# Kernel optimization log

Measured on AMD Instinct MI355X. Metric: run time of the kernel, lower is better.

Reference implementation:

```python
import jax, jax.numpy as jnp
import numpy as np

N_HOSTS = 16
N_WINDOW = 3
GAT_IN = 3
D = 16          # d_model = gat_output_feats = n_hosts
NHEAD = 2
HD = D // NHEAD # 8
FF = 64
PROTO_DIM = 8
LATENT = N_HOSTS * D * N_WINDOW  # 768
LN_EPS = 1e-5


def _positional_encoding():
    pos = np.arange(N_WINDOW, dtype=np.float32)[:, None]
    div = np.exp(np.arange(0, D, 2, dtype=np.float32) * (-np.log(10000.0) / D))
    pe = np.zeros((N_WINDOW, D), dtype=np.float32)
    pe[:, 0::2] = np.sin(pos * div)
    pe[:, 1::2] = np.cos(pos * div)
    return jnp.asarray(pe[:, None, :])  # (n_window, 1, d_model)


def setup_inputs() -> dict:
    key = jax.random.key(0)
    ks = iter(jax.random.split(key, 40))
    p = lambda *s: jax.random.normal(next(ks), s, dtype=jnp.float32) * 0.05
    inp = {
        't': jax.random.normal(next(ks), (N_WINDOW * N_HOSTS * GAT_IN,), dtype=jnp.float32),
        's': jax.random.normal(next(ks), (N_HOSTS, PROTO_DIM), dtype=jnp.float32),
        # GAT (single head, fully connected 16-node graph)
        'gat_W': p(GAT_IN, D), 'gat_a_src': p(D), 'gat_a_dst': p(D),
        # time encoder Linear(16,16)
        'te_W': p(D, D), 'te_b': p(D),
        'pe': _positional_encoding(),
        # 2 transformer encoder layers, stacked on leading axis
        'qkv_W': p(2, 3 * D, D), 'qkv_b': p(2, 3 * D),
        'out_W': p(2, D, D), 'out_b': p(2, D),
        'ln1_g': jnp.ones((2, D), jnp.float32), 'ln1_b': jnp.zeros((2, D), jnp.float32),
        'ff1_W': p(2, FF, D), 'ff1_b': p(2, FF),
        'ff2_W': p(2, D, FF), 'ff2_b': p(2, D),
        'ln2_g': jnp.ones((2, D), jnp.float32), 'ln2_b': jnp.zeros((2, D), jnp.float32),
        # decoder heads
        'an_W': p(2 * N_HOSTS, LATENT), 'an_b': p(2 * N_HOSTS),
        'pr_W': p(PROTO_DIM * N_HOSTS, LATENT), 'pr_b': p(PROTO_DIM * N_HOSTS),
    }
    return inp


def _layer_norm(x, g, b):
    m = x.mean(-1, keepdims=True)
    v = ((x - m) ** 2).mean(-1, keepdims=True)
    return (x - m) * jax.lax.rsqrt(v + LN_EPS) * g + b


def reference(t, s, gat_W, gat_a_src, gat_a_dst, te_W, te_b, pe,
              qkv_W, qkv_b, out_W, out_b, ln1_g, ln1_b,
              ff1_W, ff1_b, ff2_W, ff2_b, ln2_g, ln2_b,
              an_W, an_b, pr_W, pr_b):
    # --- GAT over fully connected 16-host graph, per window ---
    x = t.reshape(N_WINDOW, N_HOSTS, GAT_IN)
    h = x @ gat_W                                   # (w, n, D)
    e_src = h @ gat_a_src                           # (w, n)
    e_dst = h @ gat_a_dst                           # (w, n)
    e = jax.nn.leaky_relu(e_src[:, :, None] + e_dst[:, None, :], 0.2)  # (w, src, dst)
    alpha = jax.nn.softmax(e, axis=1)               # softmax over sources, per dst
    gat_out = jax.nn.elu(jnp.einsum('wsd,wsf->wdf', alpha, h))         # (w, n, D)
    # --- time encode + positional encode (dropout = identity in eval) ---
    xe = gat_out @ te_W.T + te_b + pe               # (seq=3, batch=16, D)
    # --- 2 post-norm TransformerEncoderLayers ---
    inv_sqrt_hd = 1.0 / np.sqrt(HD).astype(np.float32)
    for l in range(2):
        qkv = xe @ qkv_W[l].T + qkv_b[l]            # (s, b, 3D)
        q, k, v = jnp.split(qkv, 3, axis=-1)
        hd = lambda z: z.reshape(N_WINDOW, N_HOSTS, NHEAD, HD).transpose(1, 2, 0, 3)  # (b,h,s,hd)
        q, k, v = hd(q), hd(k), hd(v)
        att = jax.nn.softmax(jnp.einsum('bhqd,bhkd->bhqk', q, k) * inv_sqrt_hd, axis=-1)
        ctx = jnp.einsum('bhqk,bhkd->bhqd', att, v).transpose(2, 0, 1, 3).reshape(N_WINDOW, N_HOSTS, D)
        xe = _layer_norm(xe + ctx @ out_W[l].T + out_b[l], ln1_g[l], ln1_b[l])
        ff = jax.nn.relu(xe @ ff1_W[l].T + ff1_b[l]) @ ff2_W[l].T + ff2_b[l]
        xe = _layer_norm(xe + ff, ln2_g[l], ln2_b[l])
    # --- flatten to latent (batch-major, matching permute(1,0,2).reshape) ---
    latent = xe.transpose(1, 0, 2).reshape(1, LATENT)
    # nn.LeakyReLU(True): negative_slope=True==1.0, i.e. identity (faithful to source)
    anomaly = jax.nn.leaky_relu(latent @ an_W.T + an_b, 1.0).reshape(N_HOSTS, 2)
    proto = jax.nn.sigmoid(latent @ pr_W.T + pr_b).reshape(N_HOSTS, PROTO_DIM)
    return anomaly, proto
```

## Files before the change

kernel.cpp:

```cpp
#include <hip/hip_runtime.h>
#include <hip/hip_bf16.h>


#define NW 3
#define NHOST 16
#define DM 16
#define FFD 64
#define HD 8
#define LAT 768

typedef __hip_bfloat16 bf16;
typedef __attribute__((ext_vector_type(8))) unsigned short ushort8;

__device__ __forceinline__ float u2f(unsigned short u) {
    unsigned int v = ((unsigned int)u) << 16;
    return __uint_as_float(v);
}

template<typename T> __device__ __forceinline__ float ldf(const T* p, int i);
template<> __device__ __forceinline__ float ldf<bf16>(const bf16* p, int i) { return __bfloat162float(p[i]); }
template<> __device__ __forceinline__ float ldf<float>(const float* p, int i) { return p[i]; }

template<typename T> __device__ __forceinline__ void ld8(const T* p, float* o);
template<> __device__ __forceinline__ void ld8<bf16>(const bf16* p, float* o) {
    ushort8 v = *(const ushort8*)p;
    #pragma unroll
    for (int u = 0; u < 8; ++u) o[u] = u2f(v[u]);
}
template<> __device__ __forceinline__ void ld8<float>(const float* p, float* o) {
    float4 a = ((const float4*)p)[0];
    float4 b = ((const float4*)p)[1];
    o[0] = a.x; o[1] = a.y; o[2] = a.z; o[3] = a.w;
    o[4] = b.x; o[5] = b.y; o[6] = b.z; o[7] = b.w;
}

template<typename T> __device__ __forceinline__ void stf(T* p, int i, float v);
template<> __device__ __forceinline__ void stf<bf16>(bf16* p, int i, float v) { p[i] = __float2bfloat16(v); }
template<> __device__ __forceinline__ void stf<float>(float* p, int i, float v) { p[i] = v; }

struct Smem {
    float h[NW][NHOST][DM];
    float esrc[NW][NHOST];
    float edst[NW][NHOST];
    float alpha[NW][NHOST][NHOST];
    float xe[NW][NHOST][DM];
    float qkv[NW][NHOST][48];
    float ctx[NW][NHOST][DM];
    float tmp[NW][NHOST][DM];
    float ffh[NW][NHOST][FFD];
    float latent[LAT];
};

template<typename T>
__device__ void run_model(Smem& sm, int tid,
    const T* t, const T* gat_W, const T* a_src, const T* a_dst,
    const T* te_W, const T* te_b, const T* pe,
    const T* qkv_W, const T* qkv_b, const T* out_W, const T* out_b,
    const T* ln1_g, const T* ln1_b,
    const T* ff1_W, const T* ff1_b, const T* ff2_W, const T* ff2_b,
    const T* ln2_g, const T* ln2_b,
    const T* an_W, const T* an_b, const T* pr_W, const T* pr_b,
    T* out)
{
    for (int idx = tid; idx < NW * NHOST * DM; idx += 256) {
        int w = idx >> 8, r = idx & 255, n = r >> 4, f = r & 15;
        float acc = 0.f;
        #pragma unroll
        for (int i = 0; i < 3; ++i)
            acc += ldf(t, (w * NHOST + n) * 3 + i) * ldf(gat_W, i * DM + f);
        sm.h[w][n][f] = acc;
    }
    __syncthreads();

    if (tid < 96) {
        int w = tid / 32, r = tid % 32, n = r & 15, which = r >> 4;
        const T* a = which ? a_dst : a_src;
        float acc = 0.f;
        #pragma unroll
        for (int f = 0; f < DM; ++f) acc += sm.h[w][n][f] * ldf(a, f);
        if (which) sm.edst[w][n] = acc; else sm.esrc[w][n] = acc;
    }
    __syncthreads();

    if (tid < 48) {
        int w = tid / 16, d = tid & 15;
        float ed = sm.edst[w][d];
        float e[16];
        float mx = -1e30f;
        #pragma unroll
        for (int s = 0; s < 16; ++s) {
            float x = sm.esrc[w][s] + ed;
            x = x > 0.f ? x : 0.2f * x;
            e[s] = x;
            mx = fmaxf(mx, x);
        }
        float sum = 0.f;
        #pragma unroll
        for (int s = 0; s < 16; ++s) { e[s] = __expf(e[s] - mx); sum += e[s]; }
        float inv = 1.f / sum;
        #pragma unroll
        for (int s = 0; s < 16; ++s) sm.alpha[w][s][d] = e[s] * inv;
    }
    __syncthreads();

    for (int idx = tid; idx < NW * NHOST * DM; idx += 256) {
        int w = idx >> 8, r = idx & 255, d = r >> 4, f = r & 15;
        float acc = 0.f;
        #pragma unroll
        for (int s = 0; s < 16; ++s) acc += sm.alpha[w][s][d] * sm.h[w][s][f];
        sm.tmp[w][d][f] = acc > 0.f ? acc : (__expf(acc) - 1.f);
    }
    __syncthreads();

    for (int idx = tid; idx < NW * NHOST * DM; idx += 256) {
        int w = idx >> 8, r = idx & 255, n = r >> 4, f = r & 15;
        float acc = ldf(te_b, f) + ldf(pe, w * DM + f);
        #pragma unroll
        for (int g = 0; g < DM; ++g) acc += sm.tmp[w][n][g] * ldf(te_W, f * DM + g);
        sm.xe[w][n][f] = acc;
    }
    __syncthreads();

    for (int l = 0; l < 2; ++l) {
        const T* qW = qkv_W + l * 48 * DM;
        const T* qb = qkv_b + l * 48;
        for (int idx = tid; idx < NW * NHOST * 48; idx += 256) {
            int w = idx / (NHOST * 48), r = idx % (NHOST * 48), n = r / 48, j = r % 48;
            float acc = ldf(qb, j);
            #pragma unroll
            for (int f = 0; f < DM; ++f) acc += sm.xe[w][n][f] * ldf(qW, j * DM + f);
            sm.qkv[w][n][j] = acc;
        }
        __syncthreads();

        if (tid < 96) {
            int b = tid / 6, r = tid % 6, hh = r / 3, qs = r % 3;
            const float inv_sqrt_hd = 0.35355339059327373f;
            float sc[3];
            #pragma unroll
            for (int ks = 0; ks < 3; ++ks) {
                float acc = 0.f;
                #pragma unroll
                for (int d0 = 0; d0 < HD; ++d0)
                    acc += sm.qkv[qs][b][hh * HD + d0] * sm.qkv[ks][b][16 + hh * HD + d0];
                sc[ks] = acc * inv_sqrt_hd;
            }
            float mx = fmaxf(sc[0], fmaxf(sc[1], sc[2]));
            float s0 = __expf(sc[0] - mx), s1 = __expf(sc[1] - mx), s2 = __expf(sc[2] - mx);
            float inv = 1.f / (s0 + s1 + s2);
            s0 *= inv; s1 *= inv; s2 *= inv;
            #pragma unroll
            for (int d0 = 0; d0 < HD; ++d0)
                sm.ctx[qs][b][hh * HD + d0] = s0 * sm.qkv[0][b][32 + hh * HD + d0]
                                            + s1 * sm.qkv[1][b][32 + hh * HD + d0]
                                            + s2 * sm.qkv[2][b][32 + hh * HD + d0];
        }
        __syncthreads();

        const T* oW = out_W + l * DM * DM;
        const T* ob = out_b + l * DM;
        for (int idx = tid; idx < NW * NHOST * DM; idx += 256) {
            int w = idx >> 8, r = idx & 255, n = r >> 4, f = r & 15;
            float acc = ldf(ob, f) + sm.xe[w][n][f];
            #pragma unroll
            for (int g = 0; g < DM; ++g) acc += sm.ctx[w][n][g] * ldf(oW, f * DM + g);
            sm.tmp[w][n][f] = acc;
        }
        __syncthreads();

        if (tid < 48) {
            int w = tid / 16, n = tid & 15;
            float m = 0.f;
            #pragma unroll
            for (int f = 0; f < DM; ++f) m += sm.tmp[w][n][f];
            m *= (1.f / 16.f);
            float v = 0.f;
            #pragma unroll
            for (int f = 0; f < DM; ++f) { float d0 = sm.tmp[w][n][f] - m; v += d0 * d0; }
            v *= (1.f / 16.f);
            float rr = rsqrtf(v + 1e-5f);
            #pragma unroll
            for (int f = 0; f < DM; ++f)
                sm.xe[w][n][f] = (sm.tmp[w][n][f] - m) * rr * ldf(ln1_g, l * DM + f) + ldf(ln1_b, l * DM + f);
        }
        __syncthreads();

        const T* f1W = ff1_W + l * FFD * DM;
        const T* f1b = ff1_b + l * FFD;
        for (int idx = tid; idx < NW * NHOST * FFD; idx += 256) {
            int w = idx / (NHOST * FFD), r = idx % (NHOST * FFD), n = r / FFD, j = r % FFD;
            float acc = ldf(f1b, j);
            #pragma unroll
            for (int f = 0; f < DM; ++f) acc += sm.xe[w][n][f] * ldf(f1W, j * DM + f);
            sm.ffh[w][n][j] = fmaxf(acc, 0.f);
        }
        __syncthreads();

        const T* f2W = ff2_W + l * DM * FFD;
        const T* f2b = ff2_b + l * DM;
        for (int idx = tid; idx < NW * NHOST * DM; idx += 256) {
            int w = idx >> 8, r = idx & 255, n = r >> 4, f = r & 15;
            float acc = ldf(f2b, f) + sm.xe[w][n][f];
            #pragma unroll
            for (int j = 0; j < FFD; ++j) acc += sm.ffh[w][n][j] * ldf(f2W, f * FFD + j);
            sm.tmp[w][n][f] = acc;
        }
        __syncthreads();

        if (tid < 48) {
            int w = tid / 16, n = tid & 15;
            float m = 0.f;
            #pragma unroll
            for (int f = 0; f < DM; ++f) m += sm.tmp[w][n][f];
            m *= (1.f / 16.f);
            float v = 0.f;
            #pragma unroll
            for (int f = 0; f < DM; ++f) { float d0 = sm.tmp[w][n][f] - m; v += d0 * d0; }
            v *= (1.f / 16.f);
            float rr = rsqrtf(v + 1e-5f);
            #pragma unroll
            for (int f = 0; f < DM; ++f)
                sm.xe[w][n][f] = (sm.tmp[w][n][f] - m) * rr * ldf(ln2_g, l * DM + f) + ldf(ln2_b, l * DM + f);
        }
        __syncthreads();
    }

    for (int idx = tid; idx < LAT; idx += 256) {
        int w = idx >> 8, r = idx & 255, n = r >> 4, f = r & 15;
        sm.latent[n * 48 + w * DM + f] = sm.xe[w][n][f];
    }
    __syncthreads();

    {
        int g = tid >> 4;
        int lane = tid & 15;
        int base = lane * 48;
        #pragma unroll 1
        for (int rep = 0; rep < 10; ++rep) {
            int o = rep * 16 + g;
            const T* Wr = (o < 32) ? (an_W + o * LAT) : (pr_W + (o - 32) * LAT);
            float acc = 0.f;
            #pragma unroll
            for (int c = 0; c < 6; ++c) {
                float wv[8];
                ld8(Wr + base + c * 8, wv);
                #pragma unroll
                for (int u = 0; u < 8; ++u)
                    acc += sm.latent[base + c * 8 + u] * wv[u];
            }
            #pragma unroll
            for (int m = 1; m < 16; m <<= 1)
                acc += __shfl_xor(acc, m);
            if (lane == 0) {
                if (o < 32) {
                    stf(out, o, acc + ldf(an_b, o));
                } else {
                    float z = acc + ldf(pr_b, o - 32);
                    stf(out, o, 1.f / (1.f + __expf(-z)));
                }
            }
        }
    }
}

__global__ void __launch_bounds__(256) transformer16_fused(
    const void* t, const void* gat_W, const void* a_src, const void* a_dst,
    const void* te_W, const void* te_b, const void* pe,
    const void* qkv_W, const void* qkv_b, const void* out_W, const void* out_b,
    const void* ln1_g, const void* ln1_b,
    const void* ff1_W, const void* ff1_b, const void* ff2_W, const void* ff2_b,
    const void* ln2_g, const void* ln2_b,
    const void* an_W, const void* an_b, const void* pr_W, const void* pr_b,
    void* out)
{
    __shared__ Smem sm;
    const int tid = threadIdx.x;
    unsigned w0 = *(const unsigned*)ln1_g;
    if (w0 == 0x3F803F80u) {
        run_model<bf16>(sm, tid,
            (const bf16*)t, (const bf16*)gat_W, (const bf16*)a_src, (const bf16*)a_dst,
            (const bf16*)te_W, (const bf16*)te_b, (const bf16*)pe,
            (const bf16*)qkv_W, (const bf16*)qkv_b, (const bf16*)out_W, (const bf16*)out_b,
            (const bf16*)ln1_g, (const bf16*)ln1_b,
            (const bf16*)ff1_W, (const bf16*)ff1_b, (const bf16*)ff2_W, (const bf16*)ff2_b,
            (const bf16*)ln2_g, (const bf16*)ln2_b,
            (const bf16*)an_W, (const bf16*)an_b, (const bf16*)pr_W, (const bf16*)pr_b,
            (bf16*)out);
    } else {
        run_model<float>(sm, tid,
            (const float*)t, (const float*)gat_W, (const float*)a_src, (const float*)a_dst,
            (const float*)te_W, (const float*)te_b, (const float*)pe,
            (const float*)qkv_W, (const float*)qkv_b, (const float*)out_W, (const float*)out_b,
            (const float*)ln1_g, (const float*)ln1_b,
            (const float*)ff1_W, (const float*)ff1_b, (const float*)ff2_W, (const float*)ff2_b,
            (const float*)ln2_g, (const float*)ln2_b,
            (const float*)an_W, (const float*)an_b, (const float*)pr_W, (const float*)pr_b,
            (float*)out);
    }
}

extern "C" void kernel_launch(void* const* d_in, const int* in_sizes, int n_in,
                              void* d_out, int out_size, void* d_ws, size_t ws_size,
                              hipStream_t stream) {
    transformer16_fused<<<1, 256, 0, stream>>>(
        d_in[0],
        d_in[2], d_in[3], d_in[4],
        d_in[5], d_in[6], d_in[7],
        d_in[8], d_in[9], d_in[10], d_in[11],
        d_in[12], d_in[13],
        d_in[14], d_in[15], d_in[16], d_in[17],
        d_in[18], d_in[19],
        d_in[20], d_in[21], d_in[22], d_in[23],
        d_out);
}
```

Baseline: 140.3 us.

## Stage encoder weights into LDS and split decoder heads into parallel kernel

The encoder kernel now bulk-copies all small encoder weights into shared memory with 16-byte vector loads up front, so the many dependent per-element global weight reads in each stage become LDS reads. The decoder matvec, which previously ran serially on one block, moves to a separate 160-block kernel with one wavefront per output row, reading the latent from workspace. This spreads the large an_W and pr_W weight read across many CUs but adds a second launch and a global round-trip for the latent.

```diff
diff --git a/kernel.cpp b/kernel.cpp
--- a/kernel.cpp
+++ b/kernel.cpp
@@ -6,37 +6,65 @@
 #define NHOST 16
 #define DM 16
 #define FFD 64
-#define HD 8
 #define LAT 768
 
 typedef __hip_bfloat16 bf16;
-typedef __attribute__((ext_vector_type(8))) unsigned short ushort8;
-
-__device__ __forceinline__ float u2f(unsigned short u) {
-    unsigned int v = ((unsigned int)u) << 16;
-    return __uint_as_float(v);
-}
-
-template<typename T> __device__ __forceinline__ float ldf(const T* p, int i);
-template<> __device__ __forceinline__ float ldf<bf16>(const bf16* p, int i) { return __bfloat162float(p[i]); }
-template<> __device__ __forceinline__ float ldf<float>(const float* p, int i) { return p[i]; }
-
-template<typename T> __device__ __forceinline__ void ld8(const T* p, float* o);
-template<> __device__ __forceinline__ void ld8<bf16>(const bf16* p, float* o) {
-    ushort8 v = *(const ushort8*)p;
+typedef __attribute__((ext_vector_type(8))) unsigned short ushort8v;
+typedef __attribute__((ext_vector_type(4))) unsigned short ushort4v;
+
+static __device__ __forceinline__ float u2f(unsigned short u) {
+    return __uint_as_float(((unsigned)u) << 16);
+}
+
+static __device__ __forceinline__ float lwf(const unsigned short* smW, int i) { return u2f(smW[i]); }
+static __device__ __forceinline__ float lwf(const float* smW, int i) { return smW[i]; }
+
+static __device__ __forceinline__ float gld(const bf16* p, int i) { return __bfloat162float(p[i]); }
+static __device__ __forceinline__ float gld(const float* p, int i) { return p[i]; }
+static __device__ __forceinline__ void gst(bf16* p, int i, float v) { p[i] = __float2bfloat16(v); }
+static __device__ __forceinline__ void gst(float* p, int i, float v) { p[i] = v; }
+
+static __device__ __forceinline__ void ld8g(const bf16* p, float* o) {
+    ushort8v v = *(const ushort8v*)p;
     #pragma unroll
     for (int u = 0; u < 8; ++u) o[u] = u2f(v[u]);
 }
-template<> __device__ __forceinline__ void ld8<float>(const float* p, float* o) {
-    float4 a = ((const float4*)p)[0];
-    float4 b = ((const float4*)p)[1];
-    o[0] = a.x; o[1] = a.y; o[2] = a.z; o[3] = a.w;
-    o[4] = b.x; o[5] = b.y; o[6] = b.z; o[7] = b.w;
-}
-
-template<typename T> __device__ __forceinline__ void stf(T* p, int i, float v);
-template<> __device__ __forceinline__ void stf<bf16>(bf16* p, int i, float v) { p[i] = __float2bfloat16(v); }
-template<> __device__ __forceinline__ void stf<float>(float* p, int i, float v) { p[i] = v; }
+static __device__ __forceinline__ void ld8g(const float* p, float* o) {
+    float4 a = ((const float4*)p)[0], b = ((const float4*)p)[1];
+    o[0]=a.x; o[1]=a.y; o[2]=a.z; o[3]=a.w; o[4]=b.x; o[5]=b.y; o[6]=b.z; o[7]=b.w;
+}
+static __device__ __forceinline__ void ld4g(const bf16* p, float* o) {
+    ushort4v v = *(const ushort4v*)p;
+    #pragma unroll
+    for (int u = 0; u < 4; ++u) o[u] = u2f(v[u]);
+}
+static __device__ __forceinline__ void ld4g(const float* p, float* o) {
+    float4 a = *(const float4*)p;
+    o[0]=a.x; o[1]=a.y; o[2]=a.z; o[3]=a.w;
+}
+
+enum {
+    OFF_T    = 0,
+    OFF_GATW = 144,
+    OFF_ASRC = 192,
+    OFF_ADST = 208,
+    OFF_TEW  = 224,
+    OFF_TEB  = 480,
+    OFF_PE   = 496,
+    OFF_QKVW = 544,
+    OFF_QKVB = 2080,
+    OFF_OUTW = 2176,
+    OFF_OUTB = 2688,
+    OFF_LN1G = 2720,
+    OFF_LN1B = 2752,
+    OFF_FF1W = 2784,
+    OFF_FF1B = 4832,
+    OFF_FF2W = 4960,
+    OFF_FF2B = 7008,
+    OFF_LN2G = 7040,
+    OFF_LN2B = 7072,
+    TOTAL_W  = 7104
+};
 
 struct Smem {
     float h[NW][NHOST][DM];
@@ -48,36 +76,63 @@
     float ctx[NW][NHOST][DM];
     float tmp[NW][NHOST][DM];
     float ffh[NW][NHOST][FFD];
-    float latent[LAT];
 };
 
-template<typename T>
-__device__ void run_model(Smem& sm, int tid,
-    const T* t, const T* gat_W, const T* a_src, const T* a_dst,
-    const T* te_W, const T* te_b, const T* pe,
-    const T* qkv_W, const T* qkv_b, const T* out_W, const T* out_b,
-    const T* ln1_g, const T* ln1_b,
-    const T* ff1_W, const T* ff1_b, const T* ff2_W, const T* ff2_b,
-    const T* ln2_g, const T* ln2_b,
-    const T* an_W, const T* an_b, const T* pr_W, const T* pr_b,
-    T* out)
+template<typename T, typename WT>
+__device__ void encode_impl(Smem& sm, WT* smW, int tid,
+    const T* tin, const T* gatW, const T* asrc, const T* adst,
+    const T* teW, const T* teb, const T* pe_,
+    const T* qkvW, const T* qkvb, const T* outW, const T* outb,
+    const T* ln1g, const T* ln1b,
+    const T* ff1W, const T* ff1b, const T* ff2W, const T* ff2b,
+    const T* ln2g, const T* ln2b,
+    float* latent_out)
 {
+    constexpr int EPC = 16 / (int)sizeof(T);
+    constexpr int NCHUNK = TOTAL_W / EPC;
+    for (int g = tid; g < NCHUNK; g += 256) {
+        int e = g * EPC;
+        const T* p; int base;
+        if      (e < OFF_GATW) { p = tin;   base = OFF_T; }
+        else if (e < OFF_ASRC) { p = gatW;  base = OFF_GATW; }
+        else if (e < OFF_ADST) { p = asrc;  base = OFF_ASRC; }
+        else if (e < OFF_TEW)  { p = adst;  base = OFF_ADST; }
+        else if (e < OFF_TEB)  { p = teW;   base = OFF_TEW; }
+        else if (e < OFF_PE)   { p = teb;   base = OFF_TEB; }
+        else if (e < OFF_QKVW) { p = pe_;   base = OFF_PE; }
+        else if (e < OFF_QKVB) { p = qkvW;  base = OFF_QKVW; }
+        else if (e < OFF_OUTW) { p = qkvb;  base = OFF_QKVB; }
+        else if (e < OFF_OUTB) { p = outW;  base = OFF_OUTW; }
+        else if (e < OFF_LN1G) { p = outb;  base = OFF_OUTB; }
+        else if (e < OFF_LN1B) { p = ln1g;  base = OFF_LN1G; }
+        else if (e < OFF_FF1W) { p = ln1b;  base = OFF_LN1B; }
+        else if (e < OFF_FF1B) { p = ff1W;  base = OFF_FF1W; }
+        else if (e < OFF_FF2W) { p = ff1b;  base = OFF_FF1B; }
+        else if (e < OFF_FF2B) { p = ff2W;  base = OFF_FF2W; }
+        else if (e < OFF_LN2G) { p = ff2b;  base = OFF_FF2B; }
+        else if (e < OFF_LN2B) { p = ln2g;  base = OFF_LN2G; }
+        else                   { p = ln2b;  base = OFF_LN2B; }
+        *(ushort8v*)((unsigned char*)smW + (size_t)e * sizeof(T)) =
+            *(const ushort8v*)(p + (e - base));
+    }
+    __syncthreads();
+
     for (int idx = tid; idx < NW * NHOST * DM; idx += 256) {
         int w = idx >> 8, r = idx & 255, n = r >> 4, f = r & 15;
         float acc = 0.f;
         #pragma unroll
         for (int i = 0; i < 3; ++i)
-            acc += ldf(t, (w * NHOST + n) * 3 + i) * ldf(gat_W, i * DM + f);
+            acc += lwf(smW, OFF_T + (w * NHOST + n) * 3 + i) * lwf(smW, OFF_GATW + i * DM + f);
         sm.h[w][n][f] = acc;
     }
     __syncthreads();
 
     if (tid < 96) {
         int w = tid / 32, r = tid % 32, n = r & 15, which = r >> 4;
-        const T* a = which ? a_dst : a_src;
+        int abase = which ? OFF_ADST : OFF_ASRC;
         float acc = 0.f;
         #pragma unroll
-        for (int f = 0; f < DM; ++f) acc += sm.h[w][n][f] * ldf(a, f);
+        for (int f = 0; f < DM; ++f) acc += sm.h[w][n][f] * lwf(smW, abase + f);
         if (which) sm.edst[w][n] = acc; else sm.esrc[w][n] = acc;
     }
     __syncthreads();
@@ -114,21 +169,21 @@
 
     for (int idx = tid; idx < NW * NHOST * DM; idx += 256) {
         int w = idx >> 8, r = idx & 255, n = r >> 4, f = r & 15;
-        float acc = ldf(te_b, f) + ldf(pe, w * DM + f);
-        #pragma unroll
-        for (int g = 0; g < DM; ++g) acc += sm.tmp[w][n][g] * ldf(te_W, f * DM + g);
+        float acc = lwf(smW, OFF_TEB + f) + lwf(smW, OFF_PE + w * DM + f);
+        #pragma unroll
+        for (int g = 0; g < DM; ++g)
+            acc += sm.tmp[w][n][g] * lwf(smW, OFF_TEW + f * DM + g);
         sm.xe[w][n][f] = acc;
     }
     __syncthreads();
 
     for (int l = 0; l < 2; ++l) {
-        const T* qW = qkv_W + l * 48 * DM;
-        const T* qb = qkv_b + l * 48;
+        int qW = OFF_QKVW + l * 768, qb = OFF_QKVB + l * 48;
         for (int idx = tid; idx < NW * NHOST * 48; idx += 256) {
             int w = idx / (NHOST * 48), r = idx % (NHOST * 48), n = r / 48, j = r % 48;
-            float acc = ldf(qb, j);
-            #pragma unroll
-            for (int f = 0; f < DM; ++f) acc += sm.xe[w][n][f] * ldf(qW, j * DM + f);
+            float acc = lwf(smW, qb + j);
+            #pragma unroll
+            for (int f = 0; f < DM; ++f) acc += sm.xe[w][n][f] * lwf(smW, qW + j * DM + f);
             sm.qkv[w][n][j] = acc;
         }
         __syncthreads();
@@ -141,8 +196,8 @@
             for (int ks = 0; ks < 3; ++ks) {
                 float acc = 0.f;
                 #pragma unroll
-                for (int d0 = 0; d0 < HD; ++d0)
-                    acc += sm.qkv[qs][b][hh * HD + d0] * sm.qkv[ks][b][16 + hh * HD + d0];
+                for (int d0 = 0; d0 < 8; ++d0)
+                    acc += sm.qkv[qs][b][hh * 8 + d0] * sm.qkv[ks][b][16 + hh * 8 + d0];
                 sc[ks] = acc * inv_sqrt_hd;
             }
             float mx = fmaxf(sc[0], fmaxf(sc[1], sc[2]));
@@ -150,20 +205,19 @@
             float inv = 1.f / (s0 + s1 + s2);
             s0 *= inv; s1 *= inv; s2 *= inv;
             #pragma unroll
-            for (int d0 = 0; d0 < HD; ++d0)
-                sm.ctx[qs][b][hh * HD + d0] = s0 * sm.qkv[0][b][32 + hh * HD + d0]
-                                            + s1 * sm.qkv[1][b][32 + hh * HD + d0]
-                                            + s2 * sm.qkv[2][b][32 + hh * HD + d0];
-        }
-        __syncthreads();
-
-        const T* oW = out_W + l * DM * DM;
-        const T* ob = out_b + l * DM;
+            for (int d0 = 0; d0 < 8; ++d0)
+                sm.ctx[qs][b][hh * 8 + d0] = s0 * sm.qkv[0][b][32 + hh * 8 + d0]
+                                           + s1 * sm.qkv[1][b][32 + hh * 8 + d0]
+                                           + s2 * sm.qkv[2][b][32 + hh * 8 + d0];
+        }
+        __syncthreads();
+
+        int oW = OFF_OUTW + l * 256, ob = OFF_OUTB + l * 16;
         for (int idx = tid; idx < NW * NHOST * DM; idx += 256) {
             int w = idx >> 8, r = idx & 255, n = r >> 4, f = r & 15;
-            float acc = ldf(ob, f) + sm.xe[w][n][f];
-            #pragma unroll
-            for (int g = 0; g < DM; ++g) acc += sm.ctx[w][n][g] * ldf(oW, f * DM + g);
+            float acc = lwf(smW, ob + f) + sm.xe[w][n][f];
+            #pragma unroll
+            for (int g = 0; g < DM; ++g) acc += sm.ctx[w][n][g] * lwf(smW, oW + f * DM + g);
             sm.tmp[w][n][f] = acc;
         }
         __syncthreads();
@@ -181,28 +235,27 @@
             float rr = rsqrtf(v + 1e-5f);
             #pragma unroll
             for (int f = 0; f < DM; ++f)
-                sm.xe[w][n][f] = (sm.tmp[w][n][f] - m) * rr * ldf(ln1_g, l * DM + f) + ldf(ln1_b, l * DM + f);
-        }
-        __syncthreads();
-
-        const T* f1W = ff1_W + l * FFD * DM;
-        const T* f1b = ff1_b + l * FFD;
+                sm.xe[w][n][f] = (sm.tmp[w][n][f] - m) * rr * lwf(smW, OFF_LN1G + l * DM + f)
+                               + lwf(smW, OFF_LN1B + l * DM + f);
+        }
+        __syncthreads();
+
+        int f1W = OFF_FF1W + l * 1024, f1b = OFF_FF1B + l * 64;
         for (int idx = tid; idx < NW * NHOST * FFD; idx += 256) {
             int w = idx / (NHOST * FFD), r = idx % (NHOST * FFD), n = r / FFD, j = r % FFD;
-            float acc = ldf(f1b, j);
-            #pragma unroll
-            for (int f = 0; f < DM; ++f) acc += sm.xe[w][n][f] * ldf(f1W, j * DM + f);
+            float acc = lwf(smW, f1b + j);
+            #pragma unroll
+            for (int f = 0; f < DM; ++f) acc += sm.xe[w][n][f] * lwf(smW, f1W + j * DM + f);
             sm.ffh[w][n][j] = fmaxf(acc, 0.f);
         }
         __syncthreads();
 
-        const T* f2W = ff2_W + l * DM * FFD;
-        const T* f2b = ff2_b + l * DM;
+        int f2W = OFF_FF2W + l * 1024, f2b = OFF_FF2B + l * 16;
         for (int idx = tid; idx < NW * NHOST * DM; idx += 256) {
             int w = idx >> 8, r = idx & 255, n = r >> 4, f = r & 15;
-            float acc = ldf(f2b, f) + sm.xe[w][n][f];
-            #pragma unroll
-            for (int j = 0; j < FFD; ++j) acc += sm.ffh[w][n][j] * ldf(f2W, f * FFD + j);
+            float acc = lwf(smW, f2b + f) + sm.xe[w][n][f];
+            #pragma unroll
+            for (int j = 0; j < FFD; ++j) acc += sm.ffh[w][n][j] * lwf(smW, f2W + f * FFD + j);
             sm.tmp[w][n][f] = acc;
         }
         __syncthreads();
@@ -220,89 +273,102 @@
             float rr = rsqrtf(v + 1e-5f);
             #pragma unroll
             for (int f = 0; f < DM; ++f)
-                sm.xe[w][n][f] = (sm.tmp[w][n][f] - m) * rr * ldf(ln2_g, l * DM + f) + ldf(ln2_b, l * DM + f);
+                sm.xe[w][n][f] = (sm.tmp[w][n][f] - m) * rr * lwf(smW, OFF_LN2G + l * DM + f)
+                               + lwf(smW, OFF_LN2B + l * DM + f);
         }
         __syncthreads();
     }
 
     for (int idx = tid; idx < LAT; idx += 256) {
         int w = idx >> 8, r = idx & 255, n = r >> 4, f = r & 15;
-        sm.latent[n * 48 + w * DM + f] = sm.xe[w][n][f];
-    }
-    __syncthreads();
-
-    {
-        int g = tid >> 4;
-        int lane = tid & 15;
-        int base = lane * 48;
-        #pragma unroll 1
-        for (int rep = 0; rep < 10; ++rep) {
-            int o = rep * 16 + g;
-            const T* Wr = (o < 32) ? (an_W + o * LAT) : (pr_W + (o - 32) * LAT);
-            float acc = 0.f;
-            #pragma unroll
-            for (int c = 0; c < 6; ++c) {
-                float wv[8];
-                ld8(Wr + base + c * 8, wv);
-                #pragma unroll
-                for (int u = 0; u < 8; ++u)
-                    acc += sm.latent[base + c * 8 + u] * wv[u];
-            }
-            #pragma unroll
-            for (int m = 1; m < 16; m <<= 1)
-                acc += __shfl_xor(acc, m);
-            if (lane == 0) {
-                if (o < 32) {
-                    stf(out, o, acc + ldf(an_b, o));
-                } else {
-                    float z = acc + ldf(pr_b, o - 32);
-                    stf(out, o, 1.f / (1.f + __expf(-z)));
-                }
-            }
-        }
-    }
-}
-
-__global__ void __launch_bounds__(256) transformer16_fused(
+        latent_out[n * 48 + w * DM + f] = sm.xe[w][n][f];
+    }
+}
+
+__global__ void __launch_bounds__(256) txf_encode(
     const void* t, const void* gat_W, const void* a_src, const void* a_dst,
     const void* te_W, const void* te_b, const void* pe,
     const void* qkv_W, const void* qkv_b, const void* out_W, const void* out_b,
     const void* ln1_g, const void* ln1_b,
     const void* ff1_W, const void* ff1_b, const void* ff2_W, const void* ff2_b,
     const void* ln2_g, const void* ln2_b,
-    const void* an_W, const void* an_b, const void* pr_W, const void* pr_b,
-    void* out)
+    float* latent_out)
 {
     __shared__ Smem sm;
+    __shared__ __align__(16) unsigned char wbuf[TOTAL_W * 4];
     const int tid = threadIdx.x;
     unsigned w0 = *(const unsigned*)ln1_g;
     if (w0 == 0x3F803F80u) {
-        run_model<bf16>(sm, tid,
+        encode_impl<bf16, unsigned short>(sm, (unsigned short*)wbuf, tid,
             (const bf16*)t, (const bf16*)gat_W, (const bf16*)a_src, (const bf16*)a_dst,
             (const bf16*)te_W, (const bf16*)te_b, (const bf16*)pe,
             (const bf16*)qkv_W, (const bf16*)qkv_b, (const bf16*)out_W, (const bf16*)out_b,
             (const bf16*)ln1_g, (const bf16*)ln1_b,
             (const bf16*)ff1_W, (const bf16*)ff1_b, (const bf16*)ff2_W, (const bf16*)ff2_b,
-            (const bf16*)ln2_g, (const bf16*)ln2_b,
-            (const bf16*)an_W, (const bf16*)an_b, (const bf16*)pr_W, (const bf16*)pr_b,
-            (bf16*)out);
+            (const bf16*)ln2_g, (const bf16*)ln2_b, latent_out);
     } else {
-        run_model<float>(sm, tid,
+        encode_impl<float, float>(sm, (float*)wbuf, tid,
             (const float*)t, (const float*)gat_W, (const float*)a_src, (const float*)a_dst,
             (const float*)te_W, (const float*)te_b, (const float*)pe,
             (const float*)qkv_W, (const float*)qkv_b, (const float*)out_W, (const float*)out_b,
             (const float*)ln1_g, (const float*)ln1_b,
             (const float*)ff1_W, (const float*)ff1_b, (const float*)ff2_W, (const float*)ff2_b,
-            (const float*)ln2_g, (const float*)ln2_b,
-            (const float*)an_W, (const float*)an_b, (const float*)pr_W, (const float*)pr_b,
-            (float*)out);
+            (const float*)ln2_g, (const float*)ln2_b, latent_out);
+    }
+}
+
+template<typename T>
+__device__ void decode_impl(const T* an_W, const T* an_b, const T* pr_W, const T* pr_b,
+                            const float* latent, T* out)
+{
+    const int o = blockIdx.x;
+    const int l = threadIdx.x;
+    const T* Wr = (o < 32) ? (an_W + o * LAT) : (pr_W + (o - 32) * LAT);
+
+    float wv8[8], wv4[4];
+    ld8g(Wr + l * 8, wv8);
+    ld4g(Wr + 512 + l * 4, wv4);
+    float4 a = ((const float4*)latent)[2 * l];
+    float4 b = ((const float4*)latent)[2 * l + 1];
+    float4 c = ((const float4*)(latent + 512))[l];
+
+    float acc = wv8[0]*a.x + wv8[1]*a.y + wv8[2]*a.z + wv8[3]*a.w
+              + wv8[4]*b.x + wv8[5]*b.y + wv8[6]*b.z + wv8[7]*b.w
+              + wv4[0]*c.x + wv4[1]*c.y + wv4[2]*c.z + wv4[3]*c.w;
+
+    #pragma unroll
+    for (int m = 1; m < 64; m <<= 1) acc += __shfl_xor(acc, m);
+
+    if (l == 0) {
+        if (o < 32) {
+            gst(out, o, acc + gld(an_b, o));
+        } else {
+            float z = acc + gld(pr_b, o - 32);
+            gst(out, o, 1.f / (1.f + __expf(-z)));
+        }
+    }
+}
+
+__global__ void __launch_bounds__(64) txf_decode(
+    const void* an_W, const void* an_b, const void* pr_W, const void* pr_b,
+    const void* ln1_g, const float* latent, void* out)
+{
+    unsigned w0 = *(const unsigned*)ln1_g;
+    if (w0 == 0x3F803F80u) {
+        decode_impl<bf16>((const bf16*)an_W, (const bf16*)an_b,
+                          (const bf16*)pr_W, (const bf16*)pr_b, latent, (bf16*)out);
+    } else {
+        decode_impl<float>((const float*)an_W, (const float*)an_b,
+                           (const float*)pr_W, (const float*)pr_b, latent, (float*)out);
     }
 }
 
 extern "C" void kernel_launch(void* const* d_in, const int* in_sizes, int n_in,
                               void* d_out, int out_size, void* d_ws, size_t ws_size,
                               hipStream_t stream) {
-    transformer16_fused<<<1, 256, 0, stream>>>(
+    float* latent = (float*)d_ws;
+
+    txf_encode<<<1, 256, 0, stream>>>(
         d_in[0],
         d_in[2], d_in[3], d_in[4],
         d_in[5], d_in[6], d_in[7],
@@ -310,6 +376,10 @@
         d_in[12], d_in[13],
         d_in[14], d_in[15], d_in[16], d_in[17],
         d_in[18], d_in[19],
+        latent);
+
+    txf_decode<<<160, 64, 0, stream>>>(
         d_in[20], d_in[21], d_in[22], d_in[23],
-        d_out);
-}
+        d_in[12],
+        latent, d_out);
+}
```

After: 123.5 us. 1.14x faster.
